# Optimization experiments

Measured on AMD Instinct MI355X. Metric: run time of the kernel, lower is better.

Reference implementation:

```python
import jax, jax.numpy as jnp
import numpy as np

T, B, D = 8192, 8, 512
PRIOR_COUNT = 2
EPS = 1e-5


def setup_inputs() -> dict:
    key = jax.random.key(0)
    ks = jax.random.split(key, 5)
    x = jax.random.normal(ks[0], (T, B, D), dtype=jnp.float32)
    padding_mask = jnp.zeros((B, T), dtype=bool)  # True = padded position
    prior_mean = jax.random.normal(ks[1], (D,), dtype=jnp.float32) * 0.1
    prior_logv = jax.random.normal(ks[2], (D,), dtype=jnp.float32) * 0.1
    weight = jax.random.normal(ks[3], (D,), dtype=jnp.float32) * 0.1
    bias = jax.random.normal(ks[4], (D,), dtype=jnp.float32) * 0.1
    return {"x": x, "prior_mean": prior_mean, "prior_logv": prior_logv,
            "weight": weight, "bias": bias, "padding_mask": padding_mask}


def reference(x, prior_mean, prior_logv, weight, bias, padding_mask):
    # x: (T, B, D); padding_mask: (B, T) with True = pad.
    # Per-timestep Welford running mean/variance (carried across time, skipping
    # padded steps) followed by affine normalization: the TimestepNorm forward.
    gamma = weight + 1.0
    beta = bias
    b = x.shape[1]
    count0 = jnp.full((b,), PRIOR_COUNT, dtype=x.dtype)
    mean0 = jnp.broadcast_to(prior_mean, (b, D)).astype(x.dtype)
    var0 = jnp.broadcast_to(jnp.exp(prior_logv), (b, D)).astype(x.dtype)
    mask_tb = padding_mask.T  # (T, B)

    def step(carry, inp):
        count, mean, var = carry
        xt, mt = inp                                  # xt: (B, D), mt: (B,)
        valid = (~mt).astype(xt.dtype)                # 1 if real token, 0 if pad
        c_new = count + valid
        coef = valid / c_new                          # 0 on padded steps
        delta = xt - mean
        mean_new = mean + coef[:, None] * delta
        # Welford variance update: var += (delta*(x - mean_new) - var)/count
        var_new = var + coef[:, None] * (delta * (xt - mean_new) - var)
        y = (xt - mean_new) * jax.lax.rsqrt(var_new + EPS) * gamma + beta
        return (c_new, mean_new, var_new), y

    (_, _, _), ys = jax.lax.scan(step, (count0, mean0, var0), (x, mask_tb))
    return ys  # (T, B, D), same layout as module output
```

## Files before the change

### kernel.cpp

```cpp
#include <hip/hip_runtime.h>
#include <math.h>


#define T_DIM 8192
#define B_DIM 8
#define D_DIM 512
#define NC    128
#define CT    (T_DIM / NC)
#define BD    (B_DIM * D_DIM)
#define C0    2.0f
#define EPS   1e-5f


__global__ __launch_bounds__(128) void ts_pass1(
    const float* __restrict__ x, const unsigned char* __restrict__ mask,
    float* __restrict__ s1p, float* __restrict__ s2p, float* __restrict__ cnt) {
  const int chunk = blockIdx.x;
  const int b     = blockIdx.y;
  const int tid   = threadIdx.x;
  const int t0    = chunk * CT;
  const float4* xp = (const float4*)x;

  unsigned long long mw[CT / 8];
  const unsigned long long* m8 =
      (const unsigned long long*)(mask + b * T_DIM + t0);
#pragma unroll
  for (int j = 0; j < CT / 8; ++j) mw[j] = m8[j];

  float s1x = 0.f, s1y = 0.f, s1z = 0.f, s1w = 0.f;
  float s2x = 0.f, s2y = 0.f, s2z = 0.f, s2w = 0.f;
  float c = 0.f;
#pragma unroll 8
  for (int i = 0; i < CT; ++i) {
    float valid = ((mw[i >> 3] >> ((i & 7) * 8)) & 0xffULL) ? 0.f : 1.f;
    float4 v = xp[((t0 + i) * B_DIM + b) * (D_DIM / 4) + tid];
    c += valid;
    s1x += valid * v.x; s2x += valid * v.x * v.x;
    s1y += valid * v.y; s2y += valid * v.y * v.y;
    s1z += valid * v.z; s2z += valid * v.z * v.z;
    s1w += valid * v.w; s2w += valid * v.w * v.w;
  }
  const int pidx = chunk * (BD / 4) + b * (D_DIM / 4) + tid;
  ((float4*)s1p)[pidx] = make_float4(s1x, s1y, s1z, s1w);
  ((float4*)s2p)[pidx] = make_float4(s2x, s2y, s2z, s2w);
  if (tid == 0) cnt[chunk * B_DIM + b] = c;
}

__global__ __launch_bounds__(128) void ts_pass3(
    const float* __restrict__ x, const unsigned char* __restrict__ mask,
    const float* __restrict__ pm, const float* __restrict__ plv,
    const float* __restrict__ w, const float* __restrict__ bias,
    const float* __restrict__ s1p, const float* __restrict__ s2p,
    const float* __restrict__ cnt, float* __restrict__ out) {
  const int chunk = blockIdx.x;
  const int b     = blockIdx.y;
  const int tid   = threadIdx.x;
  const int t0    = chunk * CT;

  float4 S1 = make_float4(0.f, 0.f, 0.f, 0.f);
  float4 S2 = make_float4(0.f, 0.f, 0.f, 0.f);
  float csum = 0.f;
  {
    const float4* p1 = (const float4*)s1p;
    const float4* p2 = (const float4*)s2p;
    const int col = b * (D_DIM / 4) + tid;
#pragma unroll 4
    for (int k = 0; k < chunk; ++k) {
      float4 a1 = p1[k * (BD / 4) + col];
      float4 a2 = p2[k * (BD / 4) + col];
      S1.x += a1.x; S1.y += a1.y; S1.z += a1.z; S1.w += a1.w;
      S2.x += a2.x; S2.y += a2.y; S2.z += a2.z; S2.w += a2.w;
      csum += cnt[k * B_DIM + b];
    }
  }
  float c = C0 + csum;

  float4 pm4 = ((const float4*)pm)[tid];
  float4 lv4 = ((const float4*)plv)[tid];
  float4 g4  = ((const float4*)w)[tid];
  float4 be4 = ((const float4*)bias)[tid];
  g4.x += 1.f; g4.y += 1.f; g4.z += 1.f; g4.w += 1.f;
  float M0x = C0 * pm4.x, M0y = C0 * pm4.y, M0z = C0 * pm4.z, M0w = C0 * pm4.w;
  float V2x = C0 * (__expf(lv4.x) + pm4.x * pm4.x);
  float V2y = C0 * (__expf(lv4.y) + pm4.y * pm4.y);
  float V2z = C0 * (__expf(lv4.z) + pm4.z * pm4.z);
  float V2w = C0 * (__expf(lv4.w) + pm4.w * pm4.w);

  unsigned long long mw[CT / 8];
  const unsigned long long* m8 =
      (const unsigned long long*)(mask + b * T_DIM + t0);
#pragma unroll
  for (int j = 0; j < CT / 8; ++j) mw[j] = m8[j];

  const float4* xp = (const float4*)x;
  float4* op = (float4*)out;

#pragma unroll 4
  for (int i = 0; i < CT; ++i) {
    float valid = ((mw[i >> 3] >> ((i & 7) * 8)) & 0xffULL) ? 0.f : 1.f;
    const int xi = ((t0 + i) * B_DIM + b) * (D_DIM / 4) + tid;
    float4 v = xp[xi];
    c += valid;
    float rc = __builtin_amdgcn_rcpf(c);
    float4 y;
    {
      S1.x += valid * v.x; S2.x += valid * v.x * v.x;
      float M = M0x + S1.x;
      float mean = M * rc;
      float var = (V2x + S2.x - M * M * rc) * rc;
      y.x = (v.x - mean) * __builtin_amdgcn_rsqf(var + EPS) * g4.x + be4.x;
    }
    {
      S1.y += valid * v.y; S2.y += valid * v.y * v.y;
      float M = M0y + S1.y;
      float mean = M * rc;
      float var = (V2y + S2.y - M * M * rc) * rc;
      y.y = (v.y - mean) * __builtin_amdgcn_rsqf(var + EPS) * g4.y + be4.y;
    }
    {
      S1.z += valid * v.z; S2.z += valid * v.z * v.z;
      float M = M0z + S1.z;
      float mean = M * rc;
      float var = (V2z + S2.z - M * M * rc) * rc;
      y.z = (v.z - mean) * __builtin_amdgcn_rsqf(var + EPS) * g4.z + be4.z;
    }
    {
      S1.w += valid * v.w; S2.w += valid * v.w * v.w;
      float M = M0w + S1.w;
      float mean = M * rc;
      float var = (V2w + S2.w - M * M * rc) * rc;
      y.w = (v.w - mean) * __builtin_amdgcn_rsqf(var + EPS) * g4.w + be4.w;
    }
    op[xi] = y;
  }
}

extern "C" void kernel_launch(void* const* d_in, const int* in_sizes, int n_in,
                              void* d_out, int out_size, void* d_ws, size_t ws_size,
                              hipStream_t stream) {
  const float* x    = (const float*)d_in[0];
  const float* pm   = (const float*)d_in[1];
  const float* plv  = (const float*)d_in[2];
  const float* w    = (const float*)d_in[3];
  const float* bias = (const float*)d_in[4];
  const unsigned char* mask = (const unsigned char*)d_in[5];
  float* out = (float*)d_out;

  float* s1p = (float*)d_ws;
  float* s2p = s1p + (size_t)NC * BD;
  float* cnt = s2p + (size_t)NC * BD;

  dim3 grid(NC, B_DIM);
  ts_pass1<<<grid, 128, 0, stream>>>(x, mask, s1p, s2p, cnt);
  ts_pass3<<<grid, 128, 0, stream>>>(x, mask, pm, plv, w, bias, s1p, s2p, cnt, out);
}
```

Baseline: 288.9 us.

## Add parallel exclusive-scan pass over chunk partials and raise chunk count

Adds a middle kernel that turns the per-chunk sums and counts into exclusive prefix sums with one wavefront per column, using per-lane serial sums plus shuffle scans. The final pass then reads one precomputed prefix per block instead of looping over all earlier chunks, which removes the quadratic re-read of partials. Chunk count is also raised to 512 or 256 when the workspace is large enough, giving more blocks and shorter serial time loops. The cost is an extra kernel launch and more partial traffic through memory.

Result: no change. 284.6 us (-1.5%).

```diff
diff --git a/kernel.cpp b/kernel.cpp
--- a/kernel.cpp
+++ b/kernel.cpp
@@ -5,75 +5,128 @@
 #define T_DIM 8192
 #define B_DIM 8
 #define D_DIM 512
-#define NC    128
-#define CT    (T_DIM / NC)
 #define BD    (B_DIM * D_DIM)
+#define BD4   (BD / 4)
+#define D4    (D_DIM / 4)
 #define C0    2.0f
 #define EPS   1e-5f
 
-
+__device__ __forceinline__ float4 f4add(float4 a, float4 b) {
+  return make_float4(a.x + b.x, a.y + b.y, a.z + b.z, a.w + b.w);
+}
+__device__ __forceinline__ float4 f4sub(float4 a, float4 b) {
+  return make_float4(a.x - b.x, a.y - b.y, a.z - b.z, a.w - b.w);
+}
+
+template <int NC>
 __global__ __launch_bounds__(128) void ts_pass1(
     const float* __restrict__ x, const unsigned char* __restrict__ mask,
     float* __restrict__ s1p, float* __restrict__ s2p, float* __restrict__ cnt) {
+  constexpr int CT = T_DIM / NC;
+  constexpr int NW = CT / 8;
   const int chunk = blockIdx.x;
   const int b     = blockIdx.y;
   const int tid   = threadIdx.x;
   const int t0    = chunk * CT;
   const float4* xp = (const float4*)x;
 
-  unsigned long long mw[CT / 8];
+  unsigned long long mw[NW];
   const unsigned long long* m8 =
       (const unsigned long long*)(mask + b * T_DIM + t0);
 #pragma unroll
-  for (int j = 0; j < CT / 8; ++j) mw[j] = m8[j];
-
-  float s1x = 0.f, s1y = 0.f, s1z = 0.f, s1w = 0.f;
-  float s2x = 0.f, s2y = 0.f, s2z = 0.f, s2w = 0.f;
+  for (int j = 0; j < NW; ++j) mw[j] = m8[j];
+
+  float4 s1 = make_float4(0.f, 0.f, 0.f, 0.f);
+  float4 s2 = make_float4(0.f, 0.f, 0.f, 0.f);
   float c = 0.f;
 #pragma unroll 8
   for (int i = 0; i < CT; ++i) {
     float valid = ((mw[i >> 3] >> ((i & 7) * 8)) & 0xffULL) ? 0.f : 1.f;
-    float4 v = xp[((t0 + i) * B_DIM + b) * (D_DIM / 4) + tid];
+    float4 v = xp[(t0 + i) * BD4 + b * D4 + tid];
     c += valid;
-    s1x += valid * v.x; s2x += valid * v.x * v.x;
-    s1y += valid * v.y; s2y += valid * v.y * v.y;
-    s1z += valid * v.z; s2z += valid * v.z * v.z;
-    s1w += valid * v.w; s2w += valid * v.w * v.w;
-  }
-  const int pidx = chunk * (BD / 4) + b * (D_DIM / 4) + tid;
-  ((float4*)s1p)[pidx] = make_float4(s1x, s1y, s1z, s1w);
-  ((float4*)s2p)[pidx] = make_float4(s2x, s2y, s2z, s2w);
+    s1.x += valid * v.x; s2.x += valid * v.x * v.x;
+    s1.y += valid * v.y; s2.y += valid * v.y * v.y;
+    s1.z += valid * v.z; s2.z += valid * v.z * v.z;
+    s1.w += valid * v.w; s2.w += valid * v.w * v.w;
+  }
+  const int pidx = chunk * BD4 + b * D4 + tid;
+  ((float4*)s1p)[pidx] = s1;
+  ((float4*)s2p)[pidx] = s2;
   if (tid == 0) cnt[chunk * B_DIM + b] = c;
 }
 
+template <int NC>
+__global__ __launch_bounds__(256) void ts_pass2(
+    float* __restrict__ s1p, float* __restrict__ s2p, float* __restrict__ cnt) {
+  constexpr int KPL = NC / 64;
+  const int wid  = (blockIdx.x * 256 + threadIdx.x) >> 6;
+  const int lane = threadIdx.x & 63;
+
+  if (wid < 2 * BD4) {
+    float4* base = (float4*)(wid < BD4 ? s1p : s2p);
+    const int col = wid & (BD4 - 1);
+    float4 vals[KPL];
+#pragma unroll
+    for (int j = 0; j < KPL; ++j)
+      vals[j] = base[(lane * KPL + j) * BD4 + col];
+#pragma unroll
+    for (int j = 1; j < KPL; ++j) vals[j] = f4add(vals[j], vals[j - 1]);
+    float4 tot = vals[KPL - 1];
+    float4 inc = tot;
+#pragma unroll
+    for (int off = 1; off < 64; off <<= 1) {
+      float4 o;
+      o.x = __shfl_up(inc.x, off);
+      o.y = __shfl_up(inc.y, off);
+      o.z = __shfl_up(inc.z, off);
+      o.w = __shfl_up(inc.w, off);
+      if (lane >= off) inc = f4add(inc, o);
+    }
+    float4 excl = f4sub(inc, tot);
+#pragma unroll
+    for (int j = KPL - 1; j >= 1; --j)
+      base[(lane * KPL + j) * BD4 + col] = f4add(excl, vals[j - 1]);
+    base[(lane * KPL) * BD4 + col] = excl;
+  } else if (wid < 2 * BD4 + B_DIM) {
+    const int b = wid - 2 * BD4;
+    float vals[KPL];
+#pragma unroll
+    for (int j = 0; j < KPL; ++j) vals[j] = cnt[(lane * KPL + j) * B_DIM + b];
+#pragma unroll
+    for (int j = 1; j < KPL; ++j) vals[j] += vals[j - 1];
+    float tot = vals[KPL - 1];
+    float inc = tot;
+#pragma unroll
+    for (int off = 1; off < 64; off <<= 1) {
+      float o = __shfl_up(inc, off);
+      if (lane >= off) inc += o;
+    }
+    float excl = inc - tot;
+#pragma unroll
+    for (int j = KPL - 1; j >= 1; --j)
+      cnt[(lane * KPL + j) * B_DIM + b] = excl + vals[j - 1];
+    cnt[lane * KPL * B_DIM + b] = excl;
+  }
+}
+
+template <int NC>
 __global__ __launch_bounds__(128) void ts_pass3(
     const float* __restrict__ x, const unsigned char* __restrict__ mask,
     const float* __restrict__ pm, const float* __restrict__ plv,
     const float* __restrict__ w, const float* __restrict__ bias,
-    const float* __restrict__ s1p, const float* __restrict__ s2p,
-    const float* __restrict__ cnt, float* __restrict__ out) {
+    const float* __restrict__ e1, const float* __restrict__ e2,
+    const float* __restrict__ ecnt, float* __restrict__ out) {
+  constexpr int CT = T_DIM / NC;
+  constexpr int NW = CT / 8;
   const int chunk = blockIdx.x;
   const int b     = blockIdx.y;
   const int tid   = threadIdx.x;
   const int t0    = chunk * CT;
-
-  float4 S1 = make_float4(0.f, 0.f, 0.f, 0.f);
-  float4 S2 = make_float4(0.f, 0.f, 0.f, 0.f);
-  float csum = 0.f;
-  {
-    const float4* p1 = (const float4*)s1p;
-    const float4* p2 = (const float4*)s2p;
-    const int col = b * (D_DIM / 4) + tid;
-#pragma unroll 4
-    for (int k = 0; k < chunk; ++k) {
-      float4 a1 = p1[k * (BD / 4) + col];
-      float4 a2 = p2[k * (BD / 4) + col];
-      S1.x += a1.x; S1.y += a1.y; S1.z += a1.z; S1.w += a1.w;
-      S2.x += a2.x; S2.y += a2.y; S2.z += a2.z; S2.w += a2.w;
-      csum += cnt[k * B_DIM + b];
-    }
-  }
-  float c = C0 + csum;
+  const int col   = b * D4 + tid;
+
+  float4 S1 = ((const float4*)e1)[chunk * BD4 + col];
+  float4 S2 = ((const float4*)e2)[chunk * BD4 + col];
+  float c = C0 + ecnt[chunk * B_DIM + b];
 
   float4 pm4 = ((const float4*)pm)[tid];
   float4 lv4 = ((const float4*)plv)[tid];
@@ -86,11 +139,11 @@
   float V2z = C0 * (__expf(lv4.z) + pm4.z * pm4.z);
   float V2w = C0 * (__expf(lv4.w) + pm4.w * pm4.w);
 
-  unsigned long long mw[CT / 8];
+  unsigned long long mw[NW];
   const unsigned long long* m8 =
       (const unsigned long long*)(mask + b * T_DIM + t0);
 #pragma unroll
-  for (int j = 0; j < CT / 8; ++j) mw[j] = m8[j];
+  for (int j = 0; j < NW; ++j) mw[j] = m8[j];
 
   const float4* xp = (const float4*)x;
   float4* op = (float4*)out;
@@ -98,7 +151,7 @@
 #pragma unroll 4
   for (int i = 0; i < CT; ++i) {
     float valid = ((mw[i >> 3] >> ((i & 7) * 8)) & 0xffULL) ? 0.f : 1.f;
-    const int xi = ((t0 + i) * B_DIM + b) * (D_DIM / 4) + tid;
+    const int xi = (t0 + i) * BD4 + col;
     float4 v = xp[xi];
     c += valid;
     float rc = __builtin_amdgcn_rcpf(c);
@@ -135,9 +188,25 @@
   }
 }
 
+template <int NC>
+static void run_all(const float* x, const unsigned char* mask, const float* pm,
+                    const float* plv, const float* w, const float* bias,
+                    float* out, float* ws, hipStream_t stream) {
+  float* s1p = ws;
+  float* s2p = s1p + (size_t)NC * BD;
+  float* cnt = s2p + (size_t)NC * BD;
+  dim3 grid(NC, B_DIM);
+  ts_pass1<NC><<<grid, 128, 0, stream>>>(x, mask, s1p, s2p, cnt);
+  const int scan_waves = 2 * BD4 + B_DIM;
+  const int scan_blocks = (scan_waves + 3) / 4;
+  ts_pass2<NC><<<scan_blocks, 256, 0, stream>>>(s1p, s2p, cnt);
+  ts_pass3<NC><<<grid, 128, 0, stream>>>(x, mask, pm, plv, w, bias, s1p, s2p,
+                                         cnt, out);
+}
+
 extern "C" void kernel_launch(void* const* d_in, const int* in_sizes, int n_in,
-                              void* d_out, int out_size, void* d_ws, size_t ws_size,
-                              hipStream_t stream) {
+                              void* d_out, int out_size, void* d_ws,
+                              size_t ws_size, hipStream_t stream) {
   const float* x    = (const float*)d_in[0];
   const float* pm   = (const float*)d_in[1];
   const float* plv  = (const float*)d_in[2];
@@ -145,12 +214,15 @@
   const float* bias = (const float*)d_in[4];
   const unsigned char* mask = (const unsigned char*)d_in[5];
   float* out = (float*)d_out;
-
-  float* s1p = (float*)d_ws;
-  float* s2p = s1p + (size_t)NC * BD;
-  float* cnt = s2p + (size_t)NC * BD;
-
-  dim3 grid(NC, B_DIM);
-  ts_pass1<<<grid, 128, 0, stream>>>(x, mask, s1p, s2p, cnt);
-  ts_pass3<<<grid, 128, 0, stream>>>(x, mask, pm, plv, w, bias, s1p, s2p, cnt, out);
-}
+  float* ws  = (float*)d_ws;
+
+  const size_t need512 = ((size_t)2 * 512 * BD + 512 * B_DIM) * sizeof(float);
+  const size_t need256 = ((size_t)2 * 256 * BD + 256 * B_DIM) * sizeof(float);
+  if (ws_size >= need512) {
+    run_all<512>(x, mask, pm, plv, w, bias, out, ws, stream);
+  } else if (ws_size >= need256) {
+    run_all<256>(x, mask, pm, plv, w, bias, out, ws, stream);
+  } else {
+    run_all<128>(x, mask, pm, plv, w, bias, out, ws, stream);
+  }
+}
```
